# Optimization experiments

Measured on AMD Instinct MI355X. Metric: run time of the kernel, lower is better.

Reference implementation:

```python
import jax, jax.numpy as jnp
import numpy as np

N_NODES = 100000
N_EDGES = 600000
D_IN = 128
D_OUT = 128
N_REL = 16
N_BASES = 8


def setup_inputs() -> dict:
    key = jax.random.key(0)
    ks = jax.random.split(key, 6)
    x = jax.random.normal(ks[0], (N_NODES, D_IN), dtype=jnp.float32)
    edge_index = jax.random.randint(ks[1], (2, N_EDGES), 0, N_NODES, dtype=jnp.int64)
    edge_type = jax.random.randint(ks[2], (N_EDGES,), 0, N_REL, dtype=jnp.int64)
    # xavier-uniform-ish init scales
    b_lim = float(np.sqrt(6.0 / (D_IN + D_OUT)))
    c_lim = float(np.sqrt(6.0 / (N_REL + N_BASES)))
    w_lim = float(np.sqrt(6.0 / (D_IN + D_OUT)))
    bases = jax.random.uniform(ks[3], (N_BASES, D_IN, D_OUT), jnp.float32, -b_lim, b_lim)
    coefficients = jax.random.uniform(ks[4], (N_REL, N_BASES), jnp.float32, -c_lim, c_lim)
    w_self = jax.random.uniform(ks[5], (D_OUT, D_IN), jnp.float32, -w_lim, w_lim)
    return {"x": x, "edge_index": edge_index, "edge_type": edge_type,
            "bases": bases, "coefficients": coefficients, "w_self": w_self}


def reference(x, edge_index, edge_type, bases, coefficients, w_self):
    # self loop: Linear(in, out, bias=False) -> x @ W^T
    out = x @ w_self.T  # [N, D_OUT]
    # relation weights from basis decomposition
    weights = jnp.einsum('rb,bio->rio', coefficients, bases)  # [R, D_IN, D_OUT]
    row, col = edge_index[0], edge_index[1]
    xc = x[col]  # [E, D_IN] gather of source features
    n_rel = weights.shape[0]
    msg = jnp.zeros((xc.shape[0], w_self.shape[0]), dtype=x.dtype)
    # fixed small loop over relations; masked accumulate matches per-relation grouped GEMM
    for r in range(n_rel):
        sel = (edge_type == r)[:, None]
        msg = msg + jnp.where(sel, xc @ weights[r], jnp.zeros((), x.dtype))
    # scatter-add messages to destination rows
    out = out.at[row].add(msg)
    return out
```

## Files before the change

### kernel.cpp

```cpp
#include <hip/hip_runtime.h>

#define NN 100000
#define NE 600000
#define ET (NE + NN)
#define D 128
#define NREL 16
#define SCANB 391
#define TPB 4
#define MAXTILES 10954
#define GEMMG ((MAXTILES + TPB - 1) / TPB)

typedef short short8 __attribute__((ext_vector_type(8)));
typedef float f32x4 __attribute__((ext_vector_type(4)));

#define C0 0
#define O0 20
#define CU0 40
#define T0 60

#define WT_OFF   0
#define META_OFF 557056
#define DH_OFF   557568
#define DO_OFF   957568
#define DC_OFF   1357576
#define BS_OFF   1757576
#define SCP_OFF  1759576
#define SR_OFF   7360088
#define XB_OFF   10160096
#define MSGB_OFF 35760096
#define MSGA_OFF 10160096
#define NEED_B   (MSGB_OFF + (size_t)ET * 128 * 2)
#define NEED_A   (MSGA_OFF + (size_t)ET * 128 * 2)

__device__ __forceinline__ unsigned short f2bf(float f) {
  unsigned u = __builtin_bit_cast(unsigned, f);
  u += 0x7fffu + ((u >> 16) & 1u);
  return (unsigned short)(u >> 16);
}

__global__ __launch_bounds__(256) void k_weights(const float* __restrict__ bases,
    const float* __restrict__ coef, const float* __restrict__ w_self,
    unsigned short* __restrict__ wT)
{
  int idx = blockIdx.x * 256 + threadIdx.x;
  int r = idx >> 14;
  int t = idx & 16383;
  float v;
  if (r < 16) {
    int o = t >> 7, i = t & 127;
    float acc = 0.f;
    #pragma unroll
    for (int b = 0; b < 8; ++b)
      acc += coef[r * 8 + b] * bases[b * 16384 + i * 128 + o];
    v = acc;
  } else {
    v = w_self[t];
  }
  wT[idx] = f2bf(v);
}

__global__ __launch_bounds__(256) void k_xcast(const float* __restrict__ x,
    unsigned short* __restrict__ xb)
{
  int i = blockIdx.x * 256 + threadIdx.x;
  if (i >= NN * D / 4) return;
  float4 f = *(const float4*)(x + (size_t)i * 4);
  unsigned short s0 = f2bf(f.x), s1 = f2bf(f.y), s2 = f2bf(f.z), s3 = f2bf(f.w);
  unsigned long long pk = (unsigned long long)s0 | ((unsigned long long)s1 << 16)
                        | ((unsigned long long)s2 << 32) | ((unsigned long long)s3 << 48);
  *(unsigned long long*)(xb + (size_t)i * 4) = pk;
}

__global__ __launch_bounds__(256) void k_hist(const int* __restrict__ ei,
    const int* __restrict__ et, int* __restrict__ meta, int* __restrict__ dstHist)
{
  __shared__ int h[16];
  int tid = threadIdx.x;
  if (tid < 16) h[tid] = 0;
  __syncthreads();
  for (int e = blockIdx.x * 256 + tid; e < NE; e += gridDim.x * 256) {
    atomicAdd(&h[et[e]], 1);
    atomicAdd(&dstHist[ei[e]], 1);
  }
  __syncthreads();
  if (tid < 16) atomicAdd(&meta[C0 + tid], h[tid]);
}

__global__ __launch_bounds__(256) void k_scan1(const int* __restrict__ dstHist,
    int* __restrict__ dstOff, int* __restrict__ blockSums)
{
  __shared__ int sh[256];
  int tid = threadIdx.x;
  int d = blockIdx.x * 256 + tid;
  int v = (d < NN) ? (dstHist[d] + 1) : 0;
  sh[tid] = v;
  __syncthreads();
  #pragma unroll
  for (int ofs = 1; ofs < 256; ofs <<= 1) {
    int t = (tid >= ofs) ? sh[tid - ofs] : 0;
    __syncthreads();
    sh[tid] += t;
    __syncthreads();
  }
  if (d < NN) dstOff[d] = sh[tid] - v;
  if (tid == 255) blockSums[blockIdx.x] = sh[tid];
}

__global__ __launch_bounds__(512) void k_scan2(int* __restrict__ blockSums, int* __restrict__ meta)
{
  __shared__ int sh[SCANB];
  int tid = threadIdx.x;
  if (tid < SCANB) sh[tid] = blockSums[tid];
  __syncthreads();
  if (tid == 0) {
    int run = 0;
    for (int i = 0; i < SCANB; ++i) { int c = sh[i]; sh[i] = run; run += c; }
    meta[C0 + 16] = NN;
    int off = 0, toff = 0;
    for (int r = 0; r <= 16; ++r) {
      meta[O0 + r] = off;
      meta[CU0 + r] = off;
      meta[T0 + r] = toff;
      int c = meta[C0 + r];
      off += c;
      toff += (c + 63) >> 6;
    }
    meta[O0 + 17] = off;
    meta[T0 + 17] = toff;
  }
  __syncthreads();
  if (tid < SCANB) blockSums[tid] = sh[tid];
}

__global__ __launch_bounds__(256) void k_scan3(int* __restrict__ dstOff,
    const int* __restrict__ blockSums, int* __restrict__ dstCursor,
    int2* __restrict__ sCP)
{
  int tid = threadIdx.x;
  int d = blockIdx.x * 256 + tid;
  int base = blockSums[blockIdx.x];
  if (d < NN) {
    int o = dstOff[d] + base;
    dstOff[d] = o;
    dstCursor[d] = o + 1;
    sCP[NE + d] = make_int2(d, o);
  }
  if (d == NN) dstOff[NN] = ET;
}

__global__ __launch_bounds__(256) void k_self0(int2* __restrict__ sCP, int* __restrict__ sRow)
{
  int n = blockIdx.x * 256 + threadIdx.x;
  if (n < NN) { sCP[NE + n] = make_int2(n, 0); sRow[NE + n] = n; }
}

__global__ __launch_bounds__(256) void k_scatter(const int* __restrict__ ei, const int* __restrict__ et,
    int* __restrict__ meta, int2* __restrict__ sCP, int* __restrict__ sRow,
    int* __restrict__ dstCursor, int doMsg)
{
  __shared__ int h[16], base[16], lh[16];
  int tid = threadIdx.x;
  int start = blockIdx.x * 4096;
  int end = min(NE, start + 4096);
  if (tid < 16) { h[tid] = 0; lh[tid] = 0; }
  __syncthreads();
  for (int e = start + tid; e < end; e += 256)
    atomicAdd(&h[et[e]], 1);
  __syncthreads();
  if (tid < 16) base[tid] = atomicAdd(&meta[CU0 + tid], h[tid]);
  __syncthreads();
  for (int e = start + tid; e < end; e += 256) {
    int r = et[e];
    int row = ei[e];
    int pos = base[r] + atomicAdd(&lh[r], 1);
    int slot = doMsg ? atomicAdd(&dstCursor[row], 1) : 0;
    sCP[pos] = make_int2(ei[NE + e], slot);
    if (!doMsg) sRow[pos] = row;
  }
}

__global__ __launch_bounds__(256) void k_gemm(const float* __restrict__ xf,
    const unsigned short* __restrict__ xb,
    const unsigned short* __restrict__ wT, const int* __restrict__ meta,
    const int2* __restrict__ sCP, const int* __restrict__ sRow,
    unsigned short* __restrict__ msg, float* __restrict__ out,
    int xbf, int msgmode)
{
  __shared__ short As[64 * 17 * 8];
  __shared__ int Pos[64];
  __shared__ int Rows[64];

  int ntiles = meta[T0 + 17];
  int tid = threadIdx.x;
  int lane = tid & 63, wave = tid >> 6;
  int q = lane >> 4, l15 = lane & 15;
  int m = tid >> 2, ug = tid & 3;

  int rprev = -1;
  short8 bfr[2][4];

  for (int ti = 0; ti < TPB; ++ti) {
    int b = blockIdx.x * TPB + ti;
    if (b >= ntiles) break;
    int r = 0;
    while (r < 16 && meta[T0 + r + 1] <= b) ++r;
    int tile = b - meta[T0 + r];
    int boff = meta[O0 + r];
    int e0 = boff + tile * 64;
    int nrows = min(64, boff + meta[C0 + r] - e0);

    bool valid = m < nrows;
    int e = valid ? (e0 + m) : e0;
    int2 cp = sCP[e];
    if (ug == 0) {
      Pos[m] = valid ? cp.y : 0;
      if (!msgmode) Rows[m] = valid ? sRow[e] : 0;
    }
    int c = cp.x;
    if (xbf) {
      const unsigned short* xr = xb + (size_t)c * 128;
      #pragma unroll
      for (int s = 0; s < 4; ++s) {
        int u = ug * 4 + s;
        short8 pk = (short8)(short)0;
        if (valid) pk = *(const short8*)(xr + u * 8);
        *(short8*)&As[(m * 17 + u) * 8] = pk;
      }
    } else {
      const float* xr = xf + (size_t)c * 128;
      #pragma unroll
      for (int s = 0; s < 4; ++s) {
        int u = ug * 4 + s;
        float4 f0 = make_float4(0.f, 0.f, 0.f, 0.f), f1 = f0;
        if (valid) {
          f0 = *(const float4*)(xr + u * 8);
          f1 = *(const float4*)(xr + u * 8 + 4);
        }
        short8 pk;
        pk[0] = (short)f2bf(f0.x); pk[1] = (short)f2bf(f0.y);
        pk[2] = (short)f2bf(f0.z); pk[3] = (short)f2bf(f0.w);
        pk[4] = (short)f2bf(f1.x); pk[5] = (short)f2bf(f1.y);
        pk[6] = (short)f2bf(f1.z); pk[7] = (short)f2bf(f1.w);
        *(short8*)&As[(m * 17 + u) * 8] = pk;
      }
    }
    __syncthreads();

    if (r != rprev) {
      const unsigned short* wr = wT + r * 16384;
      #pragma unroll
      for (int ns = 0; ns < 2; ++ns)
        #pragma unroll
        for (int kk = 0; kk < 4; ++kk)
          bfr[ns][kk] = *(const short8*)(wr + (wave * 32 + ns * 16 + l15) * 128 + kk * 32 + q * 8);
      rprev = r;
    }

    f32x4 acc[4][2];
    #pragma unroll
    for (int ms = 0; ms < 4; ++ms)
      #pragma unroll
      for (int ns = 0; ns < 2; ++ns)
        acc[ms][ns] = (f32x4){0.f, 0.f, 0.f, 0.f};
    #pragma unroll
    for (int kk = 0; kk < 4; ++kk) {
      short8 af[4];
      #pragma unroll
      for (int ms = 0; ms < 4; ++ms)
        af[ms] = *(const short8*)&As[((ms * 16 + l15) * 17 + kk * 4 + q) * 8];
      #pragma unroll
      for (int ms = 0; ms < 4; ++ms)
        #pragma unroll
        for (int ns = 0; ns < 2; ++ns)
          acc[ms][ns] = __builtin_amdgcn_mfma_f32_16x16x32_bf16(af[ms], bfr[ns][kk], acc[ms][ns], 0, 0, 0);
    }

    if (msgmode) {
      __syncthreads();
      #pragma unroll
      for (int ms = 0; ms < 4; ++ms)
        #pragma unroll
        for (int ns = 0; ns < 2; ++ns)
          #pragma unroll
          for (int reg = 0; reg < 4; ++reg)
            As[(ms * 16 + q * 4 + reg) * 136 + wave * 32 + ns * 16 + l15] =
                (short)f2bf(acc[ms][ns][reg]);
      __syncthreads();
      #pragma unroll
      for (int i = 0; i < 4; ++i) {
        int row = wave * 16 + i * 4 + (lane >> 4);
        short8 v = *(const short8*)&As[row * 136 + (lane & 15) * 8];
        if (row < nrows)
          *(short8*)(msg + (size_t)Pos[row] * 128 + (lane & 15) * 8) = v;
      }
      __syncthreads();
    } else {
      #pragma unroll
      for (int ms = 0; ms < 4; ++ms)
        #pragma unroll
        for (int reg = 0; reg < 4; ++reg) {
          int mrow = ms * 16 + q * 4 + reg;
          if (mrow < nrows) {
            float* op = out + (size_t)Rows[mrow] * 128 + wave * 32 + l15;
            unsafeAtomicAdd(op, acc[ms][0][reg]);
            unsafeAtomicAdd(op + 16, acc[ms][1][reg]);
          }
        }
      __syncthreads();
    }
  }
}

__global__ __launch_bounds__(256) void k_reduce(const unsigned short* __restrict__ msg,
    const int* __restrict__ dstOff, float* __restrict__ out)
{
  int d = blockIdx.x * 4 + (threadIdx.x >> 6);
  if (d >= NN) return;
  int lane = threadIdx.x & 63;
  int s = dstOff[d], e = dstOff[d + 1];
  const unsigned int* base = (const unsigned int*)msg;
  float a0 = 0.f, a1 = 0.f, b0 = 0.f, b1 = 0.f;
  int j = s;
  for (; j + 1 < e; j += 2) {
    unsigned int v0 = base[(size_t)j * 64 + lane];
    unsigned int v1 = base[(size_t)(j + 1) * 64 + lane];
    a0 += __builtin_bit_cast(float, v0 << 16);
    a1 += __builtin_bit_cast(float, v0 & 0xffff0000u);
    b0 += __builtin_bit_cast(float, v1 << 16);
    b1 += __builtin_bit_cast(float, v1 & 0xffff0000u);
  }
  if (j < e) {
    unsigned int v0 = base[(size_t)j * 64 + lane];
    a0 += __builtin_bit_cast(float, v0 << 16);
    a1 += __builtin_bit_cast(float, v0 & 0xffff0000u);
  }
  float2 w; w.x = a0 + b0; w.y = a1 + b1;
  *(float2*)(out + (size_t)d * 128 + lane * 2) = w;
}

extern "C" void kernel_launch(void* const* d_in, const int* in_sizes, int n_in,
                              void* d_out, int out_size, void* d_ws, size_t ws_size,
                              hipStream_t stream)
{
  const float* x      = (const float*)d_in[0];
  const int*   ei     = (const int*)d_in[1];
  const int*   et     = (const int*)d_in[2];
  const float* bases  = (const float*)d_in[3];
  const float* coef   = (const float*)d_in[4];
  const float* w_self = (const float*)d_in[5];
  float* out = (float*)d_out;
  char* ws = (char*)d_ws;
  unsigned short* wT = (unsigned short*)(ws + WT_OFF);
  int* meta      = (int*)(ws + META_OFF);
  int* dstHist   = (int*)(ws + DH_OFF);
  int* dstOff    = (int*)(ws + DO_OFF);
  int* dstCursor = (int*)(ws + DC_OFF);
  int* blockSums = (int*)(ws + BS_OFF);
  int2* sCP      = (int2*)(ws + SCP_OFF);
  int* sRow      = (int*)(ws + SR_OFF);
  unsigned short* xb = (unsigned short*)(ws + XB_OFF);

  const int modeB = (ws_size >= NEED_B) ? 1 : 0;
  const int modeA = (modeB || ws_size >= NEED_A) ? 1 : 0;
  unsigned short* msg = (unsigned short*)(ws + (modeB ? MSGB_OFF : MSGA_OFF));

  hipMemsetAsync(ws + META_OFF, 0, 512 + 400000, stream);
  k_weights<<<(17 * 16384) / 256, 256, 0, stream>>>(bases, coef, w_self, wT);
  if (modeB)
    k_xcast<<<(NN * D / 4 + 255) / 256, 256, 0, stream>>>(x, xb);
  k_hist<<<256, 256, 0, stream>>>(ei, et, meta, dstHist);
  if (modeA) {
    k_scan1<<<SCANB, 256, 0, stream>>>(dstHist, dstOff, blockSums);
    k_scan2<<<1, 512, 0, stream>>>(blockSums, meta);
    k_scan3<<<SCANB, 256, 0, stream>>>(dstOff, blockSums, dstCursor, sCP);
  } else {
    k_scan2<<<1, 512, 0, stream>>>(blockSums, meta);
    k_self0<<<SCANB, 256, 0, stream>>>(sCP, sRow);
    hipMemsetAsync(d_out, 0, (size_t)NN * D * 4, stream);
  }
  k_scatter<<<(NE + 4095) / 4096, 256, 0, stream>>>(ei, et, meta, sCP, sRow, dstCursor, modeA);
  k_gemm<<<GEMMG, 256, 0, stream>>>(x, xb, wT, meta, sCP, sRow, msg, out, modeB, modeA);
  if (modeA)
    k_reduce<<<(NN + 3) / 4, 256, 0, stream>>>(msg, dstOff, out);
}
```

Baseline: 334.0 us.

## Prefetch next tile gathers in GEMM, fuse prep kernels, widen reduce loads

Merges the weight-build and x-cast kernels into one launch. Adds a specialised GEMM path for bf16-x and message mode that keeps tile metadata in shared memory and prefetches the next tile's gathered rows into registers while the current tile computes. It also uses a separate epilogue buffer and double-buffered position arrays so one barrier per tile can be dropped. The reduce kernel now uses 16 lanes per destination row with 16-byte loads and stores instead of 64 lanes with 4-byte ones. The changes target launch overhead, gather latency in the GEMM, and narrow memory accesses in the reduce, at the cost of more shared memory and registers.

```diff
diff --git a/kernel.cpp b/kernel.cpp
--- a/kernel.cpp
+++ b/kernel.cpp
@@ -9,9 +9,11 @@
 #define TPB 4
 #define MAXTILES 10954
 #define GEMMG ((MAXTILES + TPB - 1) / TPB)
+#define WGRID 1088
 
 typedef short short8 __attribute__((ext_vector_type(8)));
 typedef float f32x4 __attribute__((ext_vector_type(4)));
+typedef unsigned int u32x4 __attribute__((ext_vector_type(4)));
 
 #define C0 0
 #define O0 20
@@ -38,37 +40,36 @@
   return (unsigned short)(u >> 16);
 }
 
-__global__ __launch_bounds__(256) void k_weights(const float* __restrict__ bases,
+__global__ __launch_bounds__(256) void k_prep(const float* __restrict__ bases,
     const float* __restrict__ coef, const float* __restrict__ w_self,
-    unsigned short* __restrict__ wT)
-{
-  int idx = blockIdx.x * 256 + threadIdx.x;
-  int r = idx >> 14;
-  int t = idx & 16383;
-  float v;
-  if (r < 16) {
-    int o = t >> 7, i = t & 127;
-    float acc = 0.f;
-    #pragma unroll
-    for (int b = 0; b < 8; ++b)
-      acc += coef[r * 8 + b] * bases[b * 16384 + i * 128 + o];
-    v = acc;
+    unsigned short* __restrict__ wT, const float* __restrict__ x,
+    unsigned short* __restrict__ xb)
+{
+  if (blockIdx.x < WGRID) {
+    int idx = blockIdx.x * 256 + threadIdx.x;
+    int r = idx >> 14;
+    int t = idx & 16383;
+    float v;
+    if (r < 16) {
+      int o = t >> 7, i = t & 127;
+      float acc = 0.f;
+      #pragma unroll
+      for (int b = 0; b < 8; ++b)
+        acc += coef[r * 8 + b] * bases[b * 16384 + i * 128 + o];
+      v = acc;
+    } else {
+      v = w_self[t];
+    }
+    wT[idx] = f2bf(v);
   } else {
-    v = w_self[t];
-  }
-  wT[idx] = f2bf(v);
-}
-
-__global__ __launch_bounds__(256) void k_xcast(const float* __restrict__ x,
-    unsigned short* __restrict__ xb)
-{
-  int i = blockIdx.x * 256 + threadIdx.x;
-  if (i >= NN * D / 4) return;
-  float4 f = *(const float4*)(x + (size_t)i * 4);
-  unsigned short s0 = f2bf(f.x), s1 = f2bf(f.y), s2 = f2bf(f.z), s3 = f2bf(f.w);
-  unsigned long long pk = (unsigned long long)s0 | ((unsigned long long)s1 << 16)
-                        | ((unsigned long long)s2 << 32) | ((unsigned long long)s3 << 48);
-  *(unsigned long long*)(xb + (size_t)i * 4) = pk;
+    int i = (blockIdx.x - WGRID) * 256 + threadIdx.x;
+    if (i >= NN * D / 4) return;
+    float4 f = *(const float4*)(x + (size_t)i * 4);
+    unsigned short s0 = f2bf(f.x), s1 = f2bf(f.y), s2 = f2bf(f.z), s3 = f2bf(f.w);
+    unsigned long long pk = (unsigned long long)s0 | ((unsigned long long)s1 << 16)
+                          | ((unsigned long long)s2 << 32) | ((unsigned long long)s3 << 48);
+    *(unsigned long long*)(xb + (size_t)i * 4) = pk;
+  }
 }
 
 __global__ __launch_bounds__(256) void k_hist(const int* __restrict__ ei,
@@ -187,33 +188,136 @@
     int xbf, int msgmode)
 {
   __shared__ short As[64 * 17 * 8];
-  __shared__ int Pos[64];
+  __shared__ short Es[64 * 136];
+  __shared__ int Pos2[2][64];
   __shared__ int Rows[64];
-
-  int ntiles = meta[T0 + 17];
-  int tid = threadIdx.x;
+  __shared__ int Ms[80];
+
+  int tid = threadIdx.x;
+  if (tid < 80) Ms[tid] = meta[tid];
+  __syncthreads();
+  int ntiles = Ms[T0 + 17];
+
   int lane = tid & 63, wave = tid >> 6;
   int q = lane >> 4, l15 = lane & 15;
   int m = tid >> 2, ug = tid & 3;
 
+  if (xbf && msgmode) {
+    short8 pf[4];
+    int pcy = 0;
+    bool pvalid = false;
+    int r = 0, nr = 0;
+    int b = blockIdx.x * TPB;
+    if (b < ntiles) {
+      while (r < 16 && Ms[T0 + r + 1] <= b) ++r;
+      int boff = Ms[O0 + r];
+      int e0 = boff + (b - Ms[T0 + r]) * 64;
+      nr = min(64, boff + Ms[C0 + r] - e0);
+      pvalid = m < nr;
+      int2 cp = sCP[pvalid ? (e0 + m) : e0];
+      pcy = cp.y;
+      const unsigned short* xr = xb + (size_t)cp.x * 128;
+      #pragma unroll
+      for (int s = 0; s < 4; ++s) {
+        short8 v = (short8)(short)0;
+        if (pvalid) v = *(const short8*)(xr + (ug * 4 + s) * 8);
+        pf[s] = v;
+      }
+    }
+    int rprev = -1;
+    short8 bfr[2][4];
+    for (int ti = 0; ti < TPB; ++ti) {
+      b = blockIdx.x * TPB + ti;
+      if (b >= ntiles) break;
+      int curR = r, curNr = nr;
+      #pragma unroll
+      for (int s = 0; s < 4; ++s)
+        *(short8*)&As[(m * 17 + ug * 4 + s) * 8] = pf[s];
+      if (ug == 0) Pos2[ti & 1][m] = pvalid ? pcy : 0;
+      __syncthreads();
+      int bn = b + 1;
+      if (ti + 1 < TPB && bn < ntiles) {
+        int rn = curR;
+        while (rn < 16 && Ms[T0 + rn + 1] <= bn) ++rn;
+        int boff = Ms[O0 + rn];
+        int e0n = boff + (bn - Ms[T0 + rn]) * 64;
+        int nrn = min(64, boff + Ms[C0 + rn] - e0n);
+        pvalid = m < nrn;
+        int2 cp = sCP[pvalid ? (e0n + m) : e0n];
+        pcy = cp.y;
+        const unsigned short* xr = xb + (size_t)cp.x * 128;
+        #pragma unroll
+        for (int s = 0; s < 4; ++s) {
+          short8 v = (short8)(short)0;
+          if (pvalid) v = *(const short8*)(xr + (ug * 4 + s) * 8);
+          pf[s] = v;
+        }
+        r = rn; nr = nrn;
+      }
+      if (curR != rprev) {
+        const unsigned short* wr = wT + curR * 16384;
+        #pragma unroll
+        for (int ns = 0; ns < 2; ++ns)
+          #pragma unroll
+          for (int kk = 0; kk < 4; ++kk)
+            bfr[ns][kk] = *(const short8*)(wr + (wave * 32 + ns * 16 + l15) * 128 + kk * 32 + q * 8);
+        rprev = curR;
+      }
+      f32x4 acc[4][2];
+      #pragma unroll
+      for (int ms = 0; ms < 4; ++ms)
+        #pragma unroll
+        for (int ns = 0; ns < 2; ++ns)
+          acc[ms][ns] = (f32x4){0.f, 0.f, 0.f, 0.f};
+      #pragma unroll
+      for (int kk = 0; kk < 4; ++kk) {
+        short8 af[4];
+        #pragma unroll
+        for (int ms = 0; ms < 4; ++ms)
+          af[ms] = *(const short8*)&As[((ms * 16 + l15) * 17 + kk * 4 + q) * 8];
+        #pragma unroll
+        for (int ms = 0; ms < 4; ++ms)
+          #pragma unroll
+          for (int ns = 0; ns < 2; ++ns)
+            acc[ms][ns] = __builtin_amdgcn_mfma_f32_16x16x32_bf16(af[ms], bfr[ns][kk], acc[ms][ns], 0, 0, 0);
+      }
+      #pragma unroll
+      for (int ms = 0; ms < 4; ++ms)
+        #pragma unroll
+        for (int ns = 0; ns < 2; ++ns)
+          #pragma unroll
+          for (int reg = 0; reg < 4; ++reg)
+            Es[(ms * 16 + q * 4 + reg) * 136 + wave * 32 + ns * 16 + l15] =
+                (short)f2bf(acc[ms][ns][reg]);
+      __syncthreads();
+      #pragma unroll
+      for (int i = 0; i < 4; ++i) {
+        int row = wave * 16 + i * 4 + q;
+        short8 v = *(const short8*)&Es[row * 136 + l15 * 8];
+        if (row < curNr)
+          *(short8*)(msg + (size_t)Pos2[ti & 1][row] * 128 + l15 * 8) = v;
+      }
+    }
+    return;
+  }
+
   int rprev = -1;
   short8 bfr[2][4];
-
   for (int ti = 0; ti < TPB; ++ti) {
     int b = blockIdx.x * TPB + ti;
     if (b >= ntiles) break;
     int r = 0;
-    while (r < 16 && meta[T0 + r + 1] <= b) ++r;
-    int tile = b - meta[T0 + r];
-    int boff = meta[O0 + r];
+    while (r < 16 && Ms[T0 + r + 1] <= b) ++r;
+    int tile = b - Ms[T0 + r];
+    int boff = Ms[O0 + r];
     int e0 = boff + tile * 64;
-    int nrows = min(64, boff + meta[C0 + r] - e0);
+    int nrows = min(64, boff + Ms[C0 + r] - e0);
 
     bool valid = m < nrows;
     int e = valid ? (e0 + m) : e0;
     int2 cp = sCP[e];
     if (ug == 0) {
-      Pos[m] = valid ? cp.y : 0;
+      Pos2[0][m] = valid ? cp.y : 0;
       if (!msgmode) Rows[m] = valid ? sRow[e] : 0;
     }
     int c = cp.x;
@@ -283,15 +387,15 @@
         for (int ns = 0; ns < 2; ++ns)
           #pragma unroll
           for (int reg = 0; reg < 4; ++reg)
-            As[(ms * 16 + q * 4 + reg) * 136 + wave * 32 + ns * 16 + l15] =
+            Es[(ms * 16 + q * 4 + reg) * 136 + wave * 32 + ns * 16 + l15] =
                 (short)f2bf(acc[ms][ns][reg]);
       __syncthreads();
       #pragma unroll
       for (int i = 0; i < 4; ++i) {
-        int row = wave * 16 + i * 4 + (lane >> 4);
-        short8 v = *(const short8*)&As[row * 136 + (lane & 15) * 8];
+        int row = wave * 16 + i * 4 + q;
+        short8 v = *(const short8*)&Es[row * 136 + l15 * 8];
         if (row < nrows)
-          *(short8*)(msg + (size_t)Pos[row] * 128 + (lane & 15) * 8) = v;
+          *(short8*)(msg + (size_t)Pos2[0][row] * 128 + l15 * 8) = v;
       }
       __syncthreads();
     } else {
@@ -314,28 +418,40 @@
 __global__ __launch_bounds__(256) void k_reduce(const unsigned short* __restrict__ msg,
     const int* __restrict__ dstOff, float* __restrict__ out)
 {
-  int d = blockIdx.x * 4 + (threadIdx.x >> 6);
+  int d = blockIdx.x * 16 + (threadIdx.x >> 4);
   if (d >= NN) return;
-  int lane = threadIdx.x & 63;
+  int sl = threadIdx.x & 15;
   int s = dstOff[d], e = dstOff[d + 1];
-  const unsigned int* base = (const unsigned int*)msg;
-  float a0 = 0.f, a1 = 0.f, b0 = 0.f, b1 = 0.f;
+  const unsigned short* base = msg + (size_t)sl * 8;
+  float a[8], bacc[8];
+  #pragma unroll
+  for (int i = 0; i < 8; ++i) { a[i] = 0.f; bacc[i] = 0.f; }
   int j = s;
   for (; j + 1 < e; j += 2) {
-    unsigned int v0 = base[(size_t)j * 64 + lane];
-    unsigned int v1 = base[(size_t)(j + 1) * 64 + lane];
-    a0 += __builtin_bit_cast(float, v0 << 16);
-    a1 += __builtin_bit_cast(float, v0 & 0xffff0000u);
-    b0 += __builtin_bit_cast(float, v1 << 16);
-    b1 += __builtin_bit_cast(float, v1 & 0xffff0000u);
+    u32x4 v0 = *(const u32x4*)(base + (size_t)j * 128);
+    u32x4 v1 = *(const u32x4*)(base + (size_t)(j + 1) * 128);
+    #pragma unroll
+    for (int c = 0; c < 4; ++c) {
+      a[2 * c]     += __builtin_bit_cast(float, v0[c] << 16);
+      a[2 * c + 1] += __builtin_bit_cast(float, v0[c] & 0xffff0000u);
+      bacc[2 * c]     += __builtin_bit_cast(float, v1[c] << 16);
+      bacc[2 * c + 1] += __builtin_bit_cast(float, v1[c] & 0xffff0000u);
+    }
   }
   if (j < e) {
-    unsigned int v0 = base[(size_t)j * 64 + lane];
-    a0 += __builtin_bit_cast(float, v0 << 16);
-    a1 += __builtin_bit_cast(float, v0 & 0xffff0000u);
-  }
-  float2 w; w.x = a0 + b0; w.y = a1 + b1;
-  *(float2*)(out + (size_t)d * 128 + lane * 2) = w;
+    u32x4 v0 = *(const u32x4*)(base + (size_t)j * 128);
+    #pragma unroll
+    for (int c = 0; c < 4; ++c) {
+      a[2 * c]     += __builtin_bit_cast(float, v0[c] << 16);
+      a[2 * c + 1] += __builtin_bit_cast(float, v0[c] & 0xffff0000u);
+    }
+  }
+  float4 w0, w1;
+  w0.x = a[0] + bacc[0]; w0.y = a[1] + bacc[1]; w0.z = a[2] + bacc[2]; w0.w = a[3] + bacc[3];
+  w1.x = a[4] + bacc[4]; w1.y = a[5] + bacc[5]; w1.z = a[6] + bacc[6]; w1.w = a[7] + bacc[7];
+  float* op = out + (size_t)d * 128 + sl * 8;
+  *(float4*)op = w0;
+  *(float4*)(op + 4) = w1;
 }
 
 extern "C" void kernel_launch(void* const* d_in, const int* in_sizes, int n_in,
@@ -365,9 +481,7 @@
   unsigned short* msg = (unsigned short*)(ws + (modeB ? MSGB_OFF : MSGA_OFF));
 
   hipMemsetAsync(ws + META_OFF, 0, 512 + 400000, stream);
-  k_weights<<<(17 * 16384) / 256, 256, 0, stream>>>(bases, coef, w_self, wT);
-  if (modeB)
-    k_xcast<<<(NN * D / 4 + 255) / 256, 256, 0, stream>>>(x, xb);
+  k_prep<<<modeB ? (WGRID + 12500) : WGRID, 256, 0, stream>>>(bases, coef, w_self, wT, x, xb);
   k_hist<<<256, 256, 0, stream>>>(ei, et, meta, dstHist);
   if (modeA) {
     k_scan1<<<SCANB, 256, 0, stream>>>(dstHist, dstOff, blockSums);
@@ -381,5 +495,5 @@
   k_scatter<<<(NE + 4095) / 4096, 256, 0, stream>>>(ei, et, meta, sCP, sRow, dstCursor, modeA);
   k_gemm<<<GEMMG, 256, 0, stream>>>(x, xb, wT, meta, sCP, sRow, msg, out, modeB, modeA);
   if (modeA)
-    k_reduce<<<(NN + 3) / 4, 256, 0, stream>>>(msg, dstOff, out);
-}
+    k_reduce<<<(NN + 15) / 16, 256, 0, stream>>>(msg, dstOff, out);
+}
```

Result: no change. 329.5 us (-1.3%).
